# Kernel optimization log

Hardware: AMD Instinct MI355X
Metric: run time of the kernel (lower is better)

## Reference

```python
import jax, jax.numpy as jnp
import numpy as np

N = 50000   # nodes
E = 640000  # edges
D_IN = 128
D_OUT = 128
EPS = 1e-5


def _layer_norm(x, gamma, beta):
    mu = jnp.mean(x, axis=-1, keepdims=True)
    var = jnp.mean(jnp.square(x - mu), axis=-1, keepdims=True)
    return (x - mu) * jax.lax.rsqrt(var + EPS) * gamma + beta


def _sage_conv(x, src, dst, w_l, b_l, w_r):
    # PyG SAGEConv (aggr='mean', root_weight=True, normalize=False):
    #   out = lin_l(mean_{j in N(i)} x_j) + lin_r(x_i)
    msgs = x[src]                                             # [E, D]
    agg = jax.ops.segment_sum(msgs, dst, num_segments=N)      # [N, D]
    cnt = jax.ops.segment_sum(jnp.ones((E,), x.dtype), dst, num_segments=N)
    mean = agg / jnp.maximum(cnt, 1.0)[:, None]
    return mean @ w_l.T + b_l + x @ w_r.T


def setup_inputs() -> dict:
    key = jax.random.key(0)
    ks = jax.random.split(key, 12)
    s_in = 1.0 / np.sqrt(D_IN)
    s_out = 1.0 / np.sqrt(D_OUT)
    return {
        "x": jax.random.normal(ks[0], (N, D_IN), jnp.float32),
        "edges": jax.random.randint(ks[1], (2, E), 0, N),
        "dp_w": jax.random.uniform(ks[2], (D_OUT, D_IN), jnp.float32, -s_in, s_in),
        "dp_b": jnp.zeros((D_OUT,), jnp.float32),
        "sc_w": jax.random.uniform(ks[3], (D_OUT, D_IN), jnp.float32, -s_in, s_in),
        "sc_b": jnp.zeros((D_OUT,), jnp.float32),
        "g1_lw": jax.random.uniform(ks[4], (D_OUT, D_OUT), jnp.float32, -s_out, s_out),
        "g1_lb": jnp.zeros((D_OUT,), jnp.float32),
        "g1_rw": jax.random.uniform(ks[5], (D_OUT, D_OUT), jnp.float32, -s_out, s_out),
        "n1_g": jnp.ones((D_OUT,), jnp.float32),
        "n1_b": jnp.zeros((D_OUT,), jnp.float32),
        "g2_lw": jax.random.uniform(ks[6], (D_OUT, D_OUT), jnp.float32, -s_out, s_out),
        "g2_lb": jnp.zeros((D_OUT,), jnp.float32),
        "g2_rw": jax.random.uniform(ks[7], (D_OUT, D_OUT), jnp.float32, -s_out, s_out),
        "n2_g": jnp.ones((D_OUT,), jnp.float32),
        "n2_b": jnp.zeros((D_OUT,), jnp.float32),
    }


def reference(x, edges, dp_w, dp_b, sc_w, sc_b, g1_lw, g1_lb, g1_rw, n1_g, n1_b,
              g2_lw, g2_lb, g2_rw, n2_g, n2_b):
    gelu = lambda v: jax.nn.gelu(v, approximate=False)
    src, dst = edges[0], edges[1]
    shortcut = x @ sc_w.T + sc_b
    h = gelu(x @ dp_w.T + dp_b)
    h = _sage_conv(h, src, dst, g1_lw, g1_lb, g1_rw)
    h = gelu(_layer_norm(h, n1_g, n1_b))
    h = _sage_conv(h, src, dst, g2_lw, g2_lb, g2_rw)
    h = _layer_norm(h, n2_g, n2_b)
    return gelu(h + shortcut)
```

## Files before the change

kernel.cpp:

```cpp
#include <hip/hip_runtime.h>
#include <hip/hip_bf16.h>
#include <math.h>

#define D 128
#define WS 136
#define FS 132
#define PB 128

typedef __attribute__((ext_vector_type(8))) short bf16x8;
typedef __attribute__((ext_vector_type(4))) float f32x4;

__device__ __forceinline__ unsigned short f2bf(float f){
  return (unsigned short)((__float_as_uint(f) + 0x8000u) >> 16);
}
__device__ __forceinline__ float bf2f(unsigned short h){
  return __uint_as_float(((unsigned)h) << 16);
}
__device__ __forceinline__ float bf2f_lo(unsigned v){
  return __uint_as_float(v << 16);
}
__device__ __forceinline__ float bf2f_hi(unsigned v){
  return __uint_as_float(v & 0xFFFF0000u);
}
__device__ __forceinline__ float gelu_fast(float v){
  float u = v * v;
  float arg = v * (1.5957691216f + 0.0713548163f * u);
  arg = fminf(arg, 60.0f);
  float e = __expf(arg);
  return v * e * __builtin_amdgcn_rcpf(e + 1.0f);
}

__global__ __launch_bounds__(256) void k_prep(const float* s0, const float* s1,
    const float* s2, const float* s3, const float* s4, const float* s5,
    unsigned short* dst){
  int gt = blockIdx.x * 256 + threadIdx.x;
  int m = gt >> 11;
  int r = gt & 2047;
  int f = r >> 6, lane = r & 63;
  int t = f & 7, kk = f >> 3;
  int row = t * 16 + (lane & 15);
  int col = kk * 32 + (lane >> 4) * 8;
  const float* src;
  if (m == 0) src = s0; else if (m == 1) src = s1; else if (m == 2) src = s2;
  else if (m == 3) src = s3; else if (m == 4) src = s4; else src = s5;
  src += row * 128 + col;
  float4 a = *(const float4*)src;
  float4 bb = *(const float4*)(src + 4);
  bf16x8 o;
  o[0] = (short)f2bf(a.x);  o[1] = (short)f2bf(a.y);
  o[2] = (short)f2bf(a.z);  o[3] = (short)f2bf(a.w);
  o[4] = (short)f2bf(bb.x); o[5] = (short)f2bf(bb.y);
  o[6] = (short)f2bf(bb.z); o[7] = (short)f2bf(bb.w);
  int pair = m >> 1, half = m & 1;
  *(bf16x8*)(dst + (size_t)pair * 32768 + (((size_t)f * 2 + half) * 64 + lane) * 8) = o;
}

__global__ __launch_bounds__(256) void k_pcount(const int* __restrict__ edst,
    int* __restrict__ cnt, int E, int nbuck, int epb){
  __shared__ int hist[512];
  for (int b = threadIdx.x; b < nbuck; b += 256) hist[b] = 0;
  __syncthreads();
  int start = blockIdx.x * epb;
  int end = min(E, start + epb);
  for (int e = start + threadIdx.x; e < end; e += 256)
    atomicAdd(&hist[edst[e] >> 7], 1);
  __syncthreads();
  for (int b = threadIdx.x; b < nbuck; b += 256) cnt[blockIdx.x * nbuck + b] = hist[b];
}

__global__ __launch_bounds__(256) void k_pscan(const int* __restrict__ cnt,
    int* __restrict__ offs, int* __restrict__ bbase, int E, int nbuck){
  __shared__ int tot[512], base[512];
  int t = threadIdx.x;
  for (int b = t; b < nbuck; b += 256){
    int s = 0;
    for (int blk = 0; blk < PB; blk++) s += cnt[blk * nbuck + b];
    tot[b] = s;
  }
  __syncthreads();
  for (int b = t; b < nbuck; b += 256){
    int s = 0;
    for (int j = 0; j < b; j++) s += tot[j];
    base[b] = s;
  }
  __syncthreads();
  for (int b = t; b < nbuck; b += 256){
    bbase[b] = base[b];
    int run = base[b];
    for (int blk = 0; blk < PB; blk++){
      offs[blk * nbuck + b] = run;
      run += cnt[blk * nbuck + b];
    }
  }
  if (t == 0) bbase[nbuck] = E;
}

__global__ __launch_bounds__(256) void k_pscatter(const int* __restrict__ esrc,
    const int* __restrict__ edst, const int* __restrict__ offs,
    unsigned* __restrict__ ebuf, int E, int nbuck, int epb){
  __shared__ int loff[512];
  for (int b = threadIdx.x; b < nbuck; b += 256) loff[b] = offs[blockIdx.x * nbuck + b];
  __syncthreads();
  int start = blockIdx.x * epb;
  int end = min(E, start + epb);
  for (int e = start + threadIdx.x; e < end; e += 256){
    int s = esrc[e], d = edst[e];
    int b = d >> 7;
    int pos = atomicAdd(&loff[b], 1);
    ebuf[pos] = (unsigned)s | ((unsigned)(d & 127) << 16);
  }
}

__global__ __launch_bounds__(256) void k_csr(const unsigned* __restrict__ ebuf,
    const int* __restrict__ bbase, int* __restrict__ off, int* __restrict__ csr,
    int N, int E){
  __shared__ int cnt[128], pref[128], cur[128];
  int b = blockIdx.x, tid = threadIdx.x;
  int start = bbase[b], end = bbase[b + 1];
  if (tid < 128) cnt[tid] = 0;
  __syncthreads();
  for (int e = start + tid; e < end; e += 256)
    atomicAdd(&cnt[ebuf[e] >> 16], 1);
  __syncthreads();
  if (tid < 128) pref[tid] = cnt[tid];
  __syncthreads();
  for (int ofs = 1; ofs < 128; ofs <<= 1){
    int v = 0;
    if (tid < 128 && tid >= ofs) v = pref[tid - ofs];
    __syncthreads();
    if (tid < 128) pref[tid] += v;
    __syncthreads();
  }
  if (tid < 128){
    int ex = pref[tid] - cnt[tid];
    cur[tid] = ex;
    int node = b * 128 + tid;
    if (node < N) off[node] = start + ex;
  }
  if (b == 0 && tid == 0) off[N] = E;
  __syncthreads();
  for (int e = start + tid; e < end; e += 256){
    unsigned u = ebuf[e];
    int d = u >> 16;
    int p = atomicAdd(&cur[d], 1);
    csr[start + p] = (int)(u & 0xFFFFu);
  }
}

__global__ __launch_bounds__(256) void k_in(const float* __restrict__ x,
    const unsigned short* __restrict__ wp,
    const float* __restrict__ scb, const float* __restrict__ dpb,
    unsigned short* __restrict__ sbuf, unsigned short* __restrict__ hbuf, int N){
  __shared__ unsigned short tile[64 * WS];
  int tid = threadIdx.x, w = tid >> 6, lane = tid & 63, quad = lane >> 4, l16 = lane & 15;
  int nbb = blockIdx.x * 64;
  int nb = nbb + w * 16;
  int arow = min(nb + l16, N - 1);
  f32x4 acc[2][8];
  #pragma unroll
  for (int m = 0; m < 2; m++)
    #pragma unroll
    for (int t = 0; t < 8; t++) acc[m][t] = (f32x4){0.f, 0.f, 0.f, 0.f};
  #pragma unroll
  for (int kk = 0; kk < 4; kk++){
    const float* xp = x + (size_t)arow * D + kk * 32 + quad * 8;
    float4 xa = *(const float4*)xp;
    float4 xb = *(const float4*)(xp + 4);
    bf16x8 a;
    a[0] = (short)f2bf(xa.x); a[1] = (short)f2bf(xa.y);
    a[2] = (short)f2bf(xa.z); a[3] = (short)f2bf(xa.w);
    a[4] = (short)f2bf(xb.x); a[5] = (short)f2bf(xb.y);
    a[6] = (short)f2bf(xb.z); a[7] = (short)f2bf(xb.w);
    #pragma unroll
    for (int t = 0; t < 8; t++){
      size_t fo = (((size_t)(kk * 8 + t) * 2) * 64 + lane) * 8;
      bf16x8 b0 = *(const bf16x8*)(wp + fo);
      bf16x8 b1 = *(const bf16x8*)(wp + fo + 512);
      acc[0][t] = __builtin_amdgcn_mfma_f32_16x16x32_bf16(a, b0, acc[0][t], 0, 0, 0);
      acc[1][t] = __builtin_amdgcn_mfma_f32_16x16x32_bf16(a, b1, acc[1][t], 0, 0, 0);
    }
  }
  #pragma unroll
  for (int m = 0; m < 2; m++){
    const float* bias = m ? dpb : scb;
    #pragma unroll
    for (int t = 0; t < 8; t++){
      float bv = bias[t * 16 + l16];
      #pragma unroll
      for (int r = 0; r < 4; r++){
        int nl = w * 16 + quad * 4 + r;
        float v = acc[m][t][r] + bv;
        if (m) v = gelu_fast(v);
        tile[nl * WS + t * 16 + l16] = f2bf(v);
      }
    }
    __syncthreads();
    unsigned short* dst = m ? hbuf : sbuf;
    #pragma unroll
    for (int i = 0; i < 4; i++){
      int c = tid + 256 * i;
      int nl = c >> 4, j = c & 15;
      int node = nbb + nl;
      if (node < N)
        *(bf16x8*)(dst + (size_t)node * D + j * 8) = *(const bf16x8*)(tile + nl * WS + j * 8);
    }
    __syncthreads();
  }
}

__global__ __launch_bounds__(256) void k_gf(
    const unsigned short* __restrict__ hin,
    const int* __restrict__ off, const int* __restrict__ csr,
    const unsigned short* __restrict__ wp,
    const float* __restrict__ lb, const float* __restrict__ gamma,
    const float* __restrict__ beta,
    const unsigned short* __restrict__ sbuf,
    unsigned short* __restrict__ hout, float* __restrict__ fout, int N, int mode){
  extern __shared__ char smraw[];
  unsigned short* stile = (unsigned short*)smraw;
  float* ftile = (float*)smraw;
  int tid = threadIdx.x, w = tid >> 6, lane = tid & 63, quad = lane >> 4, l16 = lane & 15;
  int nbb = blockIdx.x * 64;
  int nb = nbb + w * 16;
  int node = min(nb + l16, N - 1);
  int s0 = off[node], s1 = off[node + 1];
  int deg = s1 - s0;
  float am[4][8];
  #pragma unroll
  for (int k = 0; k < 4; k++)
    #pragma unroll
    for (int c = 0; c < 8; c++) am[k][c] = 0.f;
  int j = s0;
  for (; j + 1 < s1; j += 2){
    int sA = csr[j], sB = csr[j + 1];
    const unsigned short* pA = hin + (size_t)sA * D + quad * 8;
    const unsigned short* pB = hin + (size_t)sB * D + quad * 8;
    #pragma unroll
    for (int k = 0; k < 4; k++){
      uint4 vA = *(const uint4*)(pA + k * 32);
      uint4 vB = *(const uint4*)(pB + k * 32);
      am[k][0] += bf2f_lo(vA.x) + bf2f_lo(vB.x);
      am[k][1] += bf2f_hi(vA.x) + bf2f_hi(vB.x);
      am[k][2] += bf2f_lo(vA.y) + bf2f_lo(vB.y);
      am[k][3] += bf2f_hi(vA.y) + bf2f_hi(vB.y);
      am[k][4] += bf2f_lo(vA.z) + bf2f_lo(vB.z);
      am[k][5] += bf2f_hi(vA.z) + bf2f_hi(vB.z);
      am[k][6] += bf2f_lo(vA.w) + bf2f_lo(vB.w);
      am[k][7] += bf2f_hi(vA.w) + bf2f_hi(vB.w);
    }
  }
  if (j < s1){
    int sA = csr[j];
    const unsigned short* pA = hin + (size_t)sA * D + quad * 8;
    #pragma unroll
    for (int k = 0; k < 4; k++){
      uint4 vA = *(const uint4*)(pA + k * 32);
      am[k][0] += bf2f_lo(vA.x); am[k][1] += bf2f_hi(vA.x);
      am[k][2] += bf2f_lo(vA.y); am[k][3] += bf2f_hi(vA.y);
      am[k][4] += bf2f_lo(vA.z); am[k][5] += bf2f_hi(vA.z);
      am[k][6] += bf2f_lo(vA.w); am[k][7] += bf2f_hi(vA.w);
    }
  }
  float inv = 1.0f / (float)(deg > 1 ? deg : 1);
  bf16x8 ap[4], ah[4];
  #pragma unroll
  for (int k = 0; k < 4; k++){
    ah[k] = *(const bf16x8*)(hin + (size_t)node * D + k * 32 + quad * 8);
    #pragma unroll
    for (int c = 0; c < 8; c++) ap[k][c] = (short)f2bf(am[k][c] * inv);
  }
  f32x4 acc[8];
  #pragma unroll
  for (int t = 0; t < 8; t++) acc[t] = (f32x4){0.f, 0.f, 0.f, 0.f};
  #pragma unroll
  for (int k = 0; k < 4; k++){
    #pragma unroll
    for (int t = 0; t < 8; t++){
      size_t fo = (((size_t)(k * 8 + t) * 2) * 64 + lane) * 8;
      bf16x8 bl = *(const bf16x8*)(wp + fo);
      bf16x8 br = *(const bf16x8*)(wp + fo + 512);
      acc[t] = __builtin_amdgcn_mfma_f32_16x16x32_bf16(ap[k], bl, acc[t], 0, 0, 0);
      acc[t] = __builtin_amdgcn_mfma_f32_16x16x32_bf16(ah[k], br, acc[t], 0, 0, 0);
    }
  }
  float lbv[8], gv[8], bv[8];
  #pragma unroll
  for (int t = 0; t < 8; t++){
    lbv[t] = lb[t * 16 + l16];
    gv[t] = gamma[t * 16 + l16];
    bv[t] = beta[t * 16 + l16];
  }
  float mu[4], rs[4];
  #pragma unroll
  for (int r = 0; r < 4; r++){
    float s = 0.f, qq = 0.f;
    #pragma unroll
    for (int t = 0; t < 8; t++){
      float v = acc[t][r] + lbv[t];
      acc[t][r] = v;
      s += v; qq += v * v;
    }
    s += __shfl_xor(s, 1); qq += __shfl_xor(qq, 1);
    s += __shfl_xor(s, 2); qq += __shfl_xor(qq, 2);
    s += __shfl_xor(s, 4); qq += __shfl_xor(qq, 4);
    s += __shfl_xor(s, 8); qq += __shfl_xor(qq, 8);
    float m_ = s * (1.f / 128.f);
    mu[r] = m_;
    rs[r] = rsqrtf(qq * (1.f / 128.f) - m_ * m_ + 1e-5f);
  }
  if (mode == 0){
    #pragma unroll
    for (int t = 0; t < 8; t++)
      #pragma unroll
      for (int r = 0; r < 4; r++){
        int nl = w * 16 + quad * 4 + r;
        float v = (acc[t][r] - mu[r]) * rs[r] * gv[t] + bv[t];
        stile[nl * WS + t * 16 + l16] = f2bf(gelu_fast(v));
      }
    __syncthreads();
    #pragma unroll
    for (int i = 0; i < 4; i++){
      int c = tid + 256 * i;
      int nl = c >> 4, jj = c & 15;
      int nd = nbb + nl;
      if (nd < N)
        *(bf16x8*)(hout + (size_t)nd * D + jj * 8) = *(const bf16x8*)(stile + nl * WS + jj * 8);
    }
  } else {
    #pragma unroll
    for (int i = 0; i < 4; i++){
      int c = tid + 256 * i;
      int nl = c >> 4, jj = c & 15;
      int nd = nbb + nl;
      bf16x8 v = (bf16x8){0,0,0,0,0,0,0,0};
      if (nd < N) v = *(const bf16x8*)(sbuf + (size_t)nd * D + jj * 8);
      *(bf16x8*)(stile + nl * WS + jj * 8) = v;
    }
    __syncthreads();
    float sc[8][4];
    #pragma unroll
    for (int t = 0; t < 8; t++)
      #pragma unroll
      for (int r = 0; r < 4; r++){
        int nl = w * 16 + quad * 4 + r;
        sc[t][r] = bf2f(stile[nl * WS + t * 16 + l16]);
      }
    __syncthreads();
    #pragma unroll
    for (int t = 0; t < 8; t++)
      #pragma unroll
      for (int r = 0; r < 4; r++){
        int nl = w * 16 + quad * 4 + r;
        float v = (acc[t][r] - mu[r]) * rs[r] * gv[t] + bv[t];
        ftile[nl * FS + t * 16 + l16] = gelu_fast(v + sc[t][r]);
      }
    __syncthreads();
    #pragma unroll
    for (int i = 0; i < 8; i++){
      int c = tid + 256 * i;
      int nl = c >> 5, jj = c & 31;
      int nd = nbb + nl;
      if (nd < N)
        *(float4*)(fout + (size_t)nd * D + jj * 4) = *(const float4*)(ftile + nl * FS + jj * 4);
    }
  }
}

extern "C" void kernel_launch(void* const* d_in, const int* in_sizes, int n_in,
                              void* d_out, int out_size, void* d_ws, size_t ws_size,
                              hipStream_t stream){
  const float* x     = (const float*)d_in[0];
  const int*   edges = (const int*)d_in[1];
  const float* dp_w  = (const float*)d_in[2];
  const float* dp_b  = (const float*)d_in[3];
  const float* sc_w  = (const float*)d_in[4];
  const float* sc_b  = (const float*)d_in[5];
  const float* g1_lw = (const float*)d_in[6];
  const float* g1_lb = (const float*)d_in[7];
  const float* g1_rw = (const float*)d_in[8];
  const float* n1_g  = (const float*)d_in[9];
  const float* n1_b  = (const float*)d_in[10];
  const float* g2_lw = (const float*)d_in[11];
  const float* g2_lb = (const float*)d_in[12];
  const float* g2_rw = (const float*)d_in[13];
  const float* n2_g  = (const float*)d_in[14];
  const float* n2_b  = (const float*)d_in[15];

  const int N = in_sizes[0] / D;
  const int E = in_sizes[1] / 2;
  const int* esrc = edges;
  const int* edst = edges + E;
  const int nbuck = (N + 127) >> 7;
  const int epb = (E + PB - 1) / PB;

  char* base = (char*)d_ws;
  size_t cur = 0;
  auto carve = [&](size_t b) -> char* {
    char* p = base + cur;
    cur = (cur + b + 255) & ~(size_t)255;
    return p;
  };
  unsigned* ebuf = (unsigned*)carve((size_t)E * 4);
  int* cnt       = (int*)carve((size_t)PB * nbuck * 4);
  int* offs      = (int*)carve((size_t)PB * nbuck * 4);
  int* bbase     = (int*)carve((size_t)(nbuck + 1) * 4);
  int* off       = (int*)carve((size_t)(N + 1) * 4);
  int* csr       = (int*)carve((size_t)E * 4);
  unsigned short* wb    = (unsigned short*)carve((size_t)3 * 32768 * 2);
  unsigned short* hbuf  = (unsigned short*)carve((size_t)N * D * 2);
  unsigned short* h1buf = (unsigned short*)carve((size_t)N * D * 2);
  unsigned short* sbuf  = (unsigned short*)carve((size_t)N * D * 2);

  unsigned short* wp0 = wb;
  unsigned short* wp1 = wb + 32768;
  unsigned short* wp2 = wb + 2 * 32768;

  float* out = (float*)d_out;

  k_prep<<<48, 256, 0, stream>>>(sc_w, dp_w, g1_lw, g1_rw, g2_lw, g2_rw, wb);
  k_pcount<<<PB, 256, 0, stream>>>(edst, cnt, E, nbuck, epb);
  k_pscan<<<1, 256, 0, stream>>>(cnt, offs, bbase, E, nbuck);
  k_pscatter<<<PB, 256, 0, stream>>>(esrc, edst, offs, ebuf, E, nbuck, epb);
  k_csr<<<nbuck, 256, 0, stream>>>(ebuf, bbase, off, csr, N, E);

  const int nin = (N + 63) / 64;
  k_in<<<nin, 256, 0, stream>>>(x, wp0, sc_b, dp_b, sbuf, hbuf, N);

  k_gf<<<nin, 256, 17408, stream>>>(hbuf, off, csr, wp1, g1_lb, n1_g, n1_b,
                                    nullptr, h1buf, nullptr, N, 0);
  k_gf<<<nin, 256, 33792, stream>>>(h1buf, off, csr, wp2, g2_lb, n2_g, n2_b,
                                    sbuf, nullptr, out, N, 1);
}
```

Baseline: 265.9 us.

## Split neighbor aggregation into dedicated kernel and merge independent setup kernels

```diff
diff --git a/kernel.cpp b/kernel.cpp
--- a/kernel.cpp
+++ b/kernel.cpp
@@ -30,42 +30,43 @@
   return v * e * __builtin_amdgcn_rcpf(e + 1.0f);
 }
 
-__global__ __launch_bounds__(256) void k_prep(const float* s0, const float* s1,
+__global__ __launch_bounds__(256) void k_prepcnt(const float* s0, const float* s1,
     const float* s2, const float* s3, const float* s4, const float* s5,
-    unsigned short* dst){
-  int gt = blockIdx.x * 256 + threadIdx.x;
-  int m = gt >> 11;
-  int r = gt & 2047;
-  int f = r >> 6, lane = r & 63;
-  int t = f & 7, kk = f >> 3;
-  int row = t * 16 + (lane & 15);
-  int col = kk * 32 + (lane >> 4) * 8;
-  const float* src;
-  if (m == 0) src = s0; else if (m == 1) src = s1; else if (m == 2) src = s2;
-  else if (m == 3) src = s3; else if (m == 4) src = s4; else src = s5;
-  src += row * 128 + col;
-  float4 a = *(const float4*)src;
-  float4 bb = *(const float4*)(src + 4);
-  bf16x8 o;
-  o[0] = (short)f2bf(a.x);  o[1] = (short)f2bf(a.y);
-  o[2] = (short)f2bf(a.z);  o[3] = (short)f2bf(a.w);
-  o[4] = (short)f2bf(bb.x); o[5] = (short)f2bf(bb.y);
-  o[6] = (short)f2bf(bb.z); o[7] = (short)f2bf(bb.w);
-  int pair = m >> 1, half = m & 1;
-  *(bf16x8*)(dst + (size_t)pair * 32768 + (((size_t)f * 2 + half) * 64 + lane) * 8) = o;
-}
-
-__global__ __launch_bounds__(256) void k_pcount(const int* __restrict__ edst,
-    int* __restrict__ cnt, int E, int nbuck, int epb){
+    unsigned short* dst, const int* __restrict__ edst, int* __restrict__ cnt,
+    int E, int nbuck, int epb){
   __shared__ int hist[512];
+  if (blockIdx.x < 48){
+    int gt = blockIdx.x * 256 + threadIdx.x;
+    int m = gt >> 11;
+    int r = gt & 2047;
+    int f = r >> 6, lane = r & 63;
+    int t = f & 7, kk = f >> 3;
+    int row = t * 16 + (lane & 15);
+    int col = kk * 32 + (lane >> 4) * 8;
+    const float* src;
+    if (m == 0) src = s0; else if (m == 1) src = s1; else if (m == 2) src = s2;
+    else if (m == 3) src = s3; else if (m == 4) src = s4; else src = s5;
+    src += row * 128 + col;
+    float4 a = *(const float4*)src;
+    float4 bb = *(const float4*)(src + 4);
+    bf16x8 o;
+    o[0] = (short)f2bf(a.x);  o[1] = (short)f2bf(a.y);
+    o[2] = (short)f2bf(a.z);  o[3] = (short)f2bf(a.w);
+    o[4] = (short)f2bf(bb.x); o[5] = (short)f2bf(bb.y);
+    o[6] = (short)f2bf(bb.z); o[7] = (short)f2bf(bb.w);
+    int pair = m >> 1, half = m & 1;
+    *(bf16x8*)(dst + (size_t)pair * 32768 + (((size_t)f * 2 + half) * 64 + lane) * 8) = o;
+    return;
+  }
+  int blk = blockIdx.x - 48;
   for (int b = threadIdx.x; b < nbuck; b += 256) hist[b] = 0;
   __syncthreads();
-  int start = blockIdx.x * epb;
+  int start = blk * epb;
   int end = min(E, start + epb);
   for (int e = start + threadIdx.x; e < end; e += 256)
     atomicAdd(&hist[edst[e] >> 7], 1);
   __syncthreads();
-  for (int b = threadIdx.x; b < nbuck; b += 256) cnt[blockIdx.x * nbuck + b] = hist[b];
+  for (int b = threadIdx.x; b < nbuck; b += 256) cnt[blk * nbuck + b] = hist[b];
 }
 
 __global__ __launch_bounds__(256) void k_pscan(const int* __restrict__ cnt,
@@ -111,49 +112,52 @@
   }
 }
 
-__global__ __launch_bounds__(256) void k_csr(const unsigned* __restrict__ ebuf,
-    const int* __restrict__ bbase, int* __restrict__ off, int* __restrict__ csr,
-    int N, int E){
-  __shared__ int cnt[128], pref[128], cur[128];
-  int b = blockIdx.x, tid = threadIdx.x;
-  int start = bbase[b], end = bbase[b + 1];
-  if (tid < 128) cnt[tid] = 0;
-  __syncthreads();
-  for (int e = start + tid; e < end; e += 256)
-    atomicAdd(&cnt[ebuf[e] >> 16], 1);
-  __syncthreads();
-  if (tid < 128) pref[tid] = cnt[tid];
-  __syncthreads();
-  for (int ofs = 1; ofs < 128; ofs <<= 1){
-    int v = 0;
-    if (tid < 128 && tid >= ofs) v = pref[tid - ofs];
-    __syncthreads();
-    if (tid < 128) pref[tid] += v;
-    __syncthreads();
-  }
-  if (tid < 128){
-    int ex = pref[tid] - cnt[tid];
-    cur[tid] = ex;
-    int node = b * 128 + tid;
-    if (node < N) off[node] = start + ex;
-  }
-  if (b == 0 && tid == 0) off[N] = E;
-  __syncthreads();
-  for (int e = start + tid; e < end; e += 256){
-    unsigned u = ebuf[e];
-    int d = u >> 16;
-    int p = atomicAdd(&cur[d], 1);
-    csr[start + p] = (int)(u & 0xFFFFu);
-  }
-}
-
-__global__ __launch_bounds__(256) void k_in(const float* __restrict__ x,
-    const unsigned short* __restrict__ wp,
+__global__ __launch_bounds__(256) void k_csrin(
+    const unsigned* __restrict__ ebuf, const int* __restrict__ bbase,
+    int* __restrict__ off, int* __restrict__ csr,
+    const float* __restrict__ x, const unsigned short* __restrict__ wp,
     const float* __restrict__ scb, const float* __restrict__ dpb,
-    unsigned short* __restrict__ sbuf, unsigned short* __restrict__ hbuf, int N){
+    unsigned short* __restrict__ sbuf, unsigned short* __restrict__ hbuf,
+    int N, int E, int nbuck){
+  __shared__ int cnt[128], pref[128], curs[128];
   __shared__ unsigned short tile[64 * WS];
-  int tid = threadIdx.x, w = tid >> 6, lane = tid & 63, quad = lane >> 4, l16 = lane & 15;
-  int nbb = blockIdx.x * 64;
+  int tid = threadIdx.x;
+  if ((int)blockIdx.x < nbuck){
+    int b = blockIdx.x;
+    int start = bbase[b], end = bbase[b + 1];
+    if (tid < 128) cnt[tid] = 0;
+    __syncthreads();
+    for (int e = start + tid; e < end; e += 256)
+      atomicAdd(&cnt[ebuf[e] >> 16], 1);
+    __syncthreads();
+    if (tid < 128) pref[tid] = cnt[tid];
+    __syncthreads();
+    for (int ofs = 1; ofs < 128; ofs <<= 1){
+      int v = 0;
+      if (tid < 128 && tid >= ofs) v = pref[tid - ofs];
+      __syncthreads();
+      if (tid < 128) pref[tid] += v;
+      __syncthreads();
+    }
+    if (tid < 128){
+      int ex = pref[tid] - cnt[tid];
+      curs[tid] = ex;
+      int node = b * 128 + tid;
+      if (node < N) off[node] = start + ex;
+    }
+    if (b == 0 && tid == 0) off[N] = E;
+    __syncthreads();
+    for (int e = start + tid; e < end; e += 256){
+      unsigned u = ebuf[e];
+      int d = u >> 16;
+      int p = atomicAdd(&curs[d], 1);
+      csr[start + p] = (int)(u & 0xFFFFu);
+    }
+    return;
+  }
+  int bx = blockIdx.x - nbuck;
+  int w = tid >> 6, lane = tid & 63, quad = lane >> 4, l16 = lane & 15;
+  int nbb = bx * 64;
   int nb = nbb + w * 16;
   int arow = min(nb + l16, N - 1);
   f32x4 acc[2][8];
@@ -208,9 +212,66 @@
   }
 }
 
-__global__ __launch_bounds__(256) void k_gf(
-    const unsigned short* __restrict__ hin,
+__global__ __launch_bounds__(256) void k_agg3(const unsigned short* __restrict__ h,
     const int* __restrict__ off, const int* __restrict__ csr,
+    unsigned short* __restrict__ mbuf, int N){
+  int tid = threadIdx.x;
+  int wq = tid >> 4;
+  int l16 = tid & 15;
+  int base_node = blockIdx.x * 32 + wq * 2;
+  float a[2][8];
+  #pragma unroll
+  for (int s = 0; s < 2; s++)
+    #pragma unroll
+    for (int c = 0; c < 8; c++) a[s][c] = 0.f;
+  #pragma unroll
+  for (int s = 0; s < 2; s++){
+    int node = base_node + s;
+    if (node < N){
+      int e = off[node], e1 = off[node + 1];
+      for (; e + 3 < e1; e += 4){
+        int n0 = csr[e], n1 = csr[e + 1], n2 = csr[e + 2], n3 = csr[e + 3];
+        uint4 v0 = *(const uint4*)(h + (size_t)n0 * D + l16 * 8);
+        uint4 v1 = *(const uint4*)(h + (size_t)n1 * D + l16 * 8);
+        uint4 v2 = *(const uint4*)(h + (size_t)n2 * D + l16 * 8);
+        uint4 v3 = *(const uint4*)(h + (size_t)n3 * D + l16 * 8);
+        a[s][0] += bf2f_lo(v0.x) + bf2f_lo(v1.x) + bf2f_lo(v2.x) + bf2f_lo(v3.x);
+        a[s][1] += bf2f_hi(v0.x) + bf2f_hi(v1.x) + bf2f_hi(v2.x) + bf2f_hi(v3.x);
+        a[s][2] += bf2f_lo(v0.y) + bf2f_lo(v1.y) + bf2f_lo(v2.y) + bf2f_lo(v3.y);
+        a[s][3] += bf2f_hi(v0.y) + bf2f_hi(v1.y) + bf2f_hi(v2.y) + bf2f_hi(v3.y);
+        a[s][4] += bf2f_lo(v0.z) + bf2f_lo(v1.z) + bf2f_lo(v2.z) + bf2f_lo(v3.z);
+        a[s][5] += bf2f_hi(v0.z) + bf2f_hi(v1.z) + bf2f_hi(v2.z) + bf2f_hi(v3.z);
+        a[s][6] += bf2f_lo(v0.w) + bf2f_lo(v1.w) + bf2f_lo(v2.w) + bf2f_lo(v3.w);
+        a[s][7] += bf2f_hi(v0.w) + bf2f_hi(v1.w) + bf2f_hi(v2.w) + bf2f_hi(v3.w);
+      }
+      for (; e < e1; e++){
+        int n0 = csr[e];
+        uint4 v0 = *(const uint4*)(h + (size_t)n0 * D + l16 * 8);
+        a[s][0] += bf2f_lo(v0.x); a[s][1] += bf2f_hi(v0.x);
+        a[s][2] += bf2f_lo(v0.y); a[s][3] += bf2f_hi(v0.y);
+        a[s][4] += bf2f_lo(v0.z); a[s][5] += bf2f_hi(v0.z);
+        a[s][6] += bf2f_lo(v0.w); a[s][7] += bf2f_hi(v0.w);
+      }
+    }
+  }
+  #pragma unroll
+  for (int s = 0; s < 2; s++){
+    int node = base_node + s;
+    if (node < N){
+      int deg = off[node + 1] - off[node];
+      float inv = 1.0f / (float)(deg > 1 ? deg : 1);
+      uint4 o;
+      o.x = ((unsigned)f2bf(a[s][1] * inv) << 16) | f2bf(a[s][0] * inv);
+      o.y = ((unsigned)f2bf(a[s][3] * inv) << 16) | f2bf(a[s][2] * inv);
+      o.z = ((unsigned)f2bf(a[s][5] * inv) << 16) | f2bf(a[s][4] * inv);
+      o.w = ((unsigned)f2bf(a[s][7] * inv) << 16) | f2bf(a[s][6] * inv);
+      *(uint4*)(mbuf + (size_t)node * D + l16 * 8) = o;
+    }
+  }
+}
+
+__global__ __launch_bounds__(256) void k_g(
+    const unsigned short* __restrict__ hin, const unsigned short* __restrict__ mbuf,
     const unsigned short* __restrict__ wp,
     const float* __restrict__ lb, const float* __restrict__ gamma,
     const float* __restrict__ beta,
@@ -222,65 +283,22 @@
   int tid = threadIdx.x, w = tid >> 6, lane = tid & 63, quad = lane >> 4, l16 = lane & 15;
   int nbb = blockIdx.x * 64;
   int nb = nbb + w * 16;
-  int node = min(nb + l16, N - 1);
-  int s0 = off[node], s1 = off[node + 1];
-  int deg = s1 - s0;
-  float am[4][8];
-  #pragma unroll
-  for (int k = 0; k < 4; k++)
-    #pragma unroll
-    for (int c = 0; c < 8; c++) am[k][c] = 0.f;
-  int j = s0;
-  for (; j + 1 < s1; j += 2){
-    int sA = csr[j], sB = csr[j + 1];
-    const unsigned short* pA = hin + (size_t)sA * D + quad * 8;
-    const unsigned short* pB = hin + (size_t)sB * D + quad * 8;
-    #pragma unroll
-    for (int k = 0; k < 4; k++){
-      uint4 vA = *(const uint4*)(pA + k * 32);
-      uint4 vB = *(const uint4*)(pB + k * 32);
-      am[k][0] += bf2f_lo(vA.x) + bf2f_lo(vB.x);
-      am[k][1] += bf2f_hi(vA.x) + bf2f_hi(vB.x);
-      am[k][2] += bf2f_lo(vA.y) + bf2f_lo(vB.y);
-      am[k][3] += bf2f_hi(vA.y) + bf2f_hi(vB.y);
-      am[k][4] += bf2f_lo(vA.z) + bf2f_lo(vB.z);
-      am[k][5] += bf2f_hi(vA.z) + bf2f_hi(vB.z);
-      am[k][6] += bf2f_lo(vA.w) + bf2f_lo(vB.w);
-      am[k][7] += bf2f_hi(vA.w) + bf2f_hi(vB.w);
-    }
-  }
-  if (j < s1){
-    int sA = csr[j];
-    const unsigned short* pA = hin + (size_t)sA * D + quad * 8;
-    #pragma unroll
-    for (int k = 0; k < 4; k++){
-      uint4 vA = *(const uint4*)(pA + k * 32);
-      am[k][0] += bf2f_lo(vA.x); am[k][1] += bf2f_hi(vA.x);
-      am[k][2] += bf2f_lo(vA.y); am[k][3] += bf2f_hi(vA.y);
-      am[k][4] += bf2f_lo(vA.z); am[k][5] += bf2f_hi(vA.z);
-      am[k][6] += bf2f_lo(vA.w); am[k][7] += bf2f_hi(vA.w);
-    }
-  }
-  float inv = 1.0f / (float)(deg > 1 ? deg : 1);
-  bf16x8 ap[4], ah[4];
-  #pragma unroll
-  for (int k = 0; k < 4; k++){
-    ah[k] = *(const bf16x8*)(hin + (size_t)node * D + k * 32 + quad * 8);
-    #pragma unroll
-    for (int c = 0; c < 8; c++) ap[k][c] = (short)f2bf(am[k][c] * inv);
-  }
+  int arow = min(nb + l16, N - 1);
   f32x4 acc[8];
   #pragma unroll
   for (int t = 0; t < 8; t++) acc[t] = (f32x4){0.f, 0.f, 0.f, 0.f};
   #pragma unroll
-  for (int k = 0; k < 4; k++){
+  for (int kk = 0; kk < 4; kk++){
+    int co = kk * 32 + quad * 8;
+    bf16x8 am = *(const bf16x8*)(mbuf + (size_t)arow * D + co);
+    bf16x8 ah = *(const bf16x8*)(hin + (size_t)arow * D + co);
     #pragma unroll
     for (int t = 0; t < 8; t++){
-      size_t fo = (((size_t)(k * 8 + t) * 2) * 64 + lane) * 8;
+      size_t fo = (((size_t)(kk * 8 + t) * 2) * 64 + lane) * 8;
       bf16x8 bl = *(const bf16x8*)(wp + fo);
       bf16x8 br = *(const bf16x8*)(wp + fo + 512);
-      acc[t] = __builtin_amdgcn_mfma_f32_16x16x32_bf16(ap[k], bl, acc[t], 0, 0, 0);
-      acc[t] = __builtin_amdgcn_mfma_f32_16x16x32_bf16(ah[k], br, acc[t], 0, 0, 0);
+      acc[t] = __builtin_amdgcn_mfma_f32_16x16x32_bf16(am, bl, acc[t], 0, 0, 0);
+      acc[t] = __builtin_amdgcn_mfma_f32_16x16x32_bf16(ah, br, acc[t], 0, 0, 0);
     }
   }
   float lbv[8], gv[8], bv[8];
@@ -321,20 +339,20 @@
     #pragma unroll
     for (int i = 0; i < 4; i++){
       int c = tid + 256 * i;
-      int nl = c >> 4, jj = c & 15;
-      int nd = nbb + nl;
-      if (nd < N)
-        *(bf16x8*)(hout + (size_t)nd * D + jj * 8) = *(const bf16x8*)(stile + nl * WS + jj * 8);
+      int nl = c >> 4, j = c & 15;
+      int node = nbb + nl;
+      if (node < N)
+        *(bf16x8*)(hout + (size_t)node * D + j * 8) = *(const bf16x8*)(stile + nl * WS + j * 8);
     }
   } else {
     #pragma unroll
     for (int i = 0; i < 4; i++){
       int c = tid + 256 * i;
-      int nl = c >> 4, jj = c & 15;
-      int nd = nbb + nl;
+      int nl = c >> 4, j = c & 15;
+      int node = nbb + nl;
       bf16x8 v = (bf16x8){0,0,0,0,0,0,0,0};
-      if (nd < N) v = *(const bf16x8*)(sbuf + (size_t)nd * D + jj * 8);
-      *(bf16x8*)(stile + nl * WS + jj * 8) = v;
+      if (node < N) v = *(const bf16x8*)(sbuf + (size_t)node * D + j * 8);
+      *(bf16x8*)(stile + nl * WS + j * 8) = v;
     }
     __syncthreads();
     float sc[8][4];
@@ -358,10 +376,10 @@
     #pragma unroll
     for (int i = 0; i < 8; i++){
       int c = tid + 256 * i;
-      int nl = c >> 5, jj = c & 31;
-      int nd = nbb + nl;
-      if (nd < N)
-        *(float4*)(fout + (size_t)nd * D + jj * 4) = *(const float4*)(ftile + nl * FS + jj * 4);
+      int nl = c >> 5, j = c & 31;
+      int node = nbb + nl;
+      if (node < N)
+        *(float4*)(fout + (size_t)node * D + j * 4) = *(const float4*)(ftile + nl * FS + j * 4);
     }
   }
 }
@@ -409,6 +427,7 @@
   unsigned short* wb    = (unsigned short*)carve((size_t)3 * 32768 * 2);
   unsigned short* hbuf  = (unsigned short*)carve((size_t)N * D * 2);
   unsigned short* h1buf = (unsigned short*)carve((size_t)N * D * 2);
+  unsigned short* mbuf  = (unsigned short*)carve((size_t)N * D * 2);
   unsigned short* sbuf  = (unsigned short*)carve((size_t)N * D * 2);
 
   unsigned short* wp0 = wb;
@@ -417,17 +436,21 @@
 
   float* out = (float*)d_out;
 
-  k_prep<<<48, 256, 0, stream>>>(sc_w, dp_w, g1_lw, g1_rw, g2_lw, g2_rw, wb);
-  k_pcount<<<PB, 256, 0, stream>>>(edst, cnt, E, nbuck, epb);
+  k_prepcnt<<<48 + PB, 256, 0, stream>>>(sc_w, dp_w, g1_lw, g1_rw, g2_lw, g2_rw,
+                                         wb, edst, cnt, E, nbuck, epb);
   k_pscan<<<1, 256, 0, stream>>>(cnt, offs, bbase, E, nbuck);
   k_pscatter<<<PB, 256, 0, stream>>>(esrc, edst, offs, ebuf, E, nbuck, epb);
-  k_csr<<<nbuck, 256, 0, stream>>>(ebuf, bbase, off, csr, N, E);
 
   const int nin = (N + 63) / 64;
-  k_in<<<nin, 256, 0, stream>>>(x, wp0, sc_b, dp_b, sbuf, hbuf, N);
-
-  k_gf<<<nin, 256, 17408, stream>>>(hbuf, off, csr, wp1, g1_lb, n1_g, n1_b,
-                                    nullptr, h1buf, nullptr, N, 0);
-  k_gf<<<nin, 256, 33792, stream>>>(h1buf, off, csr, wp2, g2_lb, n2_g, n2_b,
-                                    sbuf, nullptr, out, N, 1);
-}
+  k_csrin<<<nbuck + nin, 256, 0, stream>>>(ebuf, bbase, off, csr,
+                                           x, wp0, sc_b, dp_b, sbuf, hbuf,
+                                           N, E, nbuck);
+
+  const int nagg = (N + 31) / 32;
+  k_agg3<<<nagg, 256, 0, stream>>>(hbuf, off, csr, mbuf, N);
+  k_g<<<nin, 256, 17408, stream>>>(hbuf, mbuf, wp1, g1_lb, n1_g, n1_b,
+                                   nullptr, h1buf, nullptr, N, 0);
+  k_agg3<<<nagg, 256, 0, stream>>>(h1buf, off, csr, mbuf, N);
+  k_g<<<nin, 256, 33792, stream>>>(h1buf, mbuf, wp2, g2_lb, n2_g, n2_b,
+                                   sbuf, nullptr, out, N, 1);
+}
```

Result: faster. 248.1 us (-6.7%).
